# Kernel tuning notes

Hardware: AMD Instinct MI355X
Metric: run time of the kernel (lower is better)

The kernel has to match this reference:

```python
import jax, jax.numpy as jnp
import numpy as np
import math

D_MODEL = 512
N_HEADS = 8
D_K = D_MODEL // N_HEADS
B, S = 2, 4096
LN_EPS = 1e-5


def _xavier(key, fan_in, fan_out):
    limit = math.sqrt(6.0 / (fan_in + fan_out))
    return jax.random.uniform(key, (fan_in, fan_out), jnp.float32, -limit, limit)


def setup_inputs() -> dict:
    key = jax.random.key(0)
    ks = jax.random.split(key, 12)
    x = jax.random.normal(ks[0], (B, S, D_MODEL), jnp.float32)
    consciousness_state = jax.random.normal(ks[1], (B, D_MODEL), jnp.float32)
    # weights stored as [in, out] (equivalent to torch Linear weight.T)
    w_q = _xavier(ks[2], D_MODEL, D_MODEL)
    w_k = _xavier(ks[3], D_MODEL, D_MODEL)
    w_v = _xavier(ks[4], D_MODEL, D_MODEL)
    w_o = _xavier(ks[5], D_MODEL, D_MODEL)
    b_o = jnp.zeros((D_MODEL,), jnp.float32)
    w_gate = _xavier(ks[6], D_MODEL, N_HEADS)
    b_gate = jnp.zeros((N_HEADS,), jnp.float32)
    w_int = _xavier(ks[7], D_MODEL, D_MODEL)
    b_int = jnp.zeros((D_MODEL,), jnp.float32)
    ln_gamma = jnp.ones((D_MODEL,), jnp.float32)
    ln_beta = jnp.zeros((D_MODEL,), jnp.float32)
    return {"x": x, "consciousness_state": consciousness_state,
            "w_q": w_q, "w_k": w_k, "w_v": w_v, "w_o": w_o, "b_o": b_o,
            "w_gate": w_gate, "b_gate": b_gate, "w_int": w_int, "b_int": b_int,
            "ln_gamma": ln_gamma, "ln_beta": ln_beta}


def reference(x, consciousness_state, w_q, w_k, w_v, w_o, b_o,
              w_gate, b_gate, w_int, b_int, ln_gamma, ln_beta):
    b, s, d = x.shape
    # project and split heads: [B, H, S, d_k]
    def heads(w):
        return (x @ w).reshape(b, s, N_HEADS, D_K).transpose(0, 2, 1, 3)
    Q, K, V = heads(w_q), heads(w_k), heads(w_v)
    scores = jnp.einsum('bhsd,bhtd->bhst', Q, K) / math.sqrt(D_K)  # [B,H,S,S]
    # per-head consciousness gate BEFORE softmax
    cw = jax.nn.sigmoid(consciousness_state @ w_gate + b_gate)  # [B,H]
    scores = scores * cw[:, :, None, None]
    attn = jax.nn.softmax(scores, axis=-1)
    # dropout is identity in eval mode
    context = jnp.einsum('bhst,bhtd->bhsd', attn, V)
    context = context.transpose(0, 2, 1, 3).reshape(b, s, d)
    out = context @ w_o + b_o
    iw = jax.nn.sigmoid(consciousness_state @ w_int + b_int)  # [B,D]
    out = out * iw[:, None, :]
    # residual + LayerNorm
    h = out + x
    mu = jnp.mean(h, axis=-1, keepdims=True)
    var = jnp.var(h, axis=-1, keepdims=True)
    out = (h - mu) * jax.lax.rsqrt(var + LN_EPS) * ln_gamma + ln_beta
    return out, attn.mean(axis=1)
```

## Files before the change

### kernel.cpp

```cpp
#include <hip/hip_runtime.h>
#include <hip/hip_bf16.h>

using short8 = __attribute__((ext_vector_type(8))) short;
using f32x4  = __attribute__((ext_vector_type(4))) float;

#define S_LEN 4096
#define DM 512

__device__ __forceinline__ unsigned short f2b(float f) {
    unsigned int u = __float_as_uint(f);
    u += 0x7fffu + ((u >> 16) & 1u);
    return (unsigned short)(u >> 16);
}

__device__ __forceinline__ short8 pack8(float4 a, float4 b) {
    short8 r;
    r[0] = (short)f2b(a.x); r[1] = (short)f2b(a.y); r[2] = (short)f2b(a.z); r[3] = (short)f2b(a.w);
    r[4] = (short)f2b(b.x); r[5] = (short)f2b(b.y); r[6] = (short)f2b(b.z); r[7] = (short)f2b(b.w);
    return r;
}

__global__ __launch_bounds__(256) void convert_w(
    const float* __restrict__ w0, const float* __restrict__ w1,
    const float* __restrict__ w2, const float* __restrict__ w3,
    unsigned short* __restrict__ t0, unsigned short* __restrict__ t1,
    unsigned short* __restrict__ t2, unsigned short* __restrict__ t3)
{
    __shared__ float sh[64][65];
    const float* src; unsigned short* dst;
    switch (blockIdx.z) {
        case 0: src = w0; dst = t0; break;
        case 1: src = w1; dst = t1; break;
        case 2: src = w2; dst = t2; break;
        default: src = w3; dst = t3; break;
    }
    int k0 = blockIdx.x * 64, n0 = blockIdx.y * 64;
    int tid = threadIdx.x;
    for (int i = tid; i < 4096; i += 256) {
        int k = i >> 6, n = i & 63;
        sh[k][n] = src[(size_t)(k0 + k) * DM + n0 + n];
    }
    __syncthreads();
    for (int i = tid; i < 4096; i += 256) {
        int n = i >> 6, k = i & 63;
        dst[(size_t)(n0 + n) * DM + k0 + k] = f2b(sh[k][n]);
    }
}

__global__ __launch_bounds__(256) void convert_x(
    const float* __restrict__ x, unsigned short* __restrict__ xb)
{
    size_t i = ((size_t)blockIdx.x * 256 + threadIdx.x) * 8;
    float4 a = *reinterpret_cast<const float4*>(x + i);
    float4 b = *reinterpret_cast<const float4*>(x + i + 4);
    *reinterpret_cast<short8*>(xb + i) = pack8(a, b);
}

__global__ __launch_bounds__(64) void gates_kernel(
    const float* __restrict__ cs, const float* __restrict__ wg, const float* __restrict__ bg,
    const float* __restrict__ wi, const float* __restrict__ bi,
    float* __restrict__ cwout, float* __restrict__ iwout)
{
    int o = blockIdx.x, b = blockIdx.y, lane = threadIdx.x;
    const float* c = cs + (size_t)b * DM;
    float acc = 0.f;
    if (o < 8) {
        #pragma unroll
        for (int j = 0; j < 8; ++j) { int k = j * 64 + lane; acc += c[k] * wg[(size_t)k * 8 + o]; }
    } else {
        int n = o - 8;
        #pragma unroll
        for (int j = 0; j < 8; ++j) { int k = j * 64 + lane; acc += c[k] * wi[(size_t)k * DM + n]; }
    }
    #pragma unroll
    for (int d = 32; d; d >>= 1) acc += __shfl_xor(acc, d);
    if (lane == 0) {
        if (o < 8) cwout[b * 8 + o] = 1.f / (1.f + __expf(-(acc + bg[o])));
        else       iwout[b * DM + (o - 8)] = 1.f / (1.f + __expf(-(acc + bi[o - 8])));
    }
}

__global__ __launch_bounds__(256) void gemm_qkv(
    const unsigned short* __restrict__ A, const unsigned short* __restrict__ WT,
    const float* __restrict__ cw,
    unsigned short* __restrict__ Qb, unsigned short* __restrict__ Kb,
    unsigned short* __restrict__ Vt)
{
    __shared__ unsigned short a_sh[64][72];
    __shared__ unsigned short b_sh[64][72];
    const int m0 = blockIdx.x * 64;
    const int n0g = blockIdx.y * 64;
    const int which = blockIdx.y >> 3;
    const int tid = threadIdx.x;
    const int wave = tid >> 6, lane = tid & 63;
    const int g = lane >> 4, lr = lane & 15;
    const int srow = tid >> 3, skc = (tid & 7) * 8;

    float sq = 1.f;
    if (which == 0) {
        int b = blockIdx.x >> 6;
        int h = blockIdx.y & 7;
        sq = cw[b * 8 + h] * 0.125f * 1.44269504f;
    }

    f32x4 acc[4];
    #pragma unroll
    for (int i = 0; i < 4; ++i) acc[i] = (f32x4){0.f, 0.f, 0.f, 0.f};

    short8 ar[2], br[2];
    #pragma unroll
    for (int cc = 0; cc < 2; ++cc) {
        int row = srow + cc * 32;
        ar[cc] = *reinterpret_cast<const short8*>(A  + (size_t)(m0  + row) * DM + skc);
        br[cc] = *reinterpret_cast<const short8*>(WT + (size_t)(n0g + row) * DM + skc);
    }

    for (int k0 = 0; k0 < 512; k0 += 64) {
        #pragma unroll
        for (int cc = 0; cc < 2; ++cc) {
            int row = srow + cc * 32;
            *reinterpret_cast<short8*>(&a_sh[row][skc]) = ar[cc];
            *reinterpret_cast<short8*>(&b_sh[row][skc]) = br[cc];
        }
        __syncthreads();
        if (k0 + 64 < 512) {
            #pragma unroll
            for (int cc = 0; cc < 2; ++cc) {
                int row = srow + cc * 32;
                ar[cc] = *reinterpret_cast<const short8*>(A  + (size_t)(m0  + row) * DM + k0 + 64 + skc);
                br[cc] = *reinterpret_cast<const short8*>(WT + (size_t)(n0g + row) * DM + k0 + 64 + skc);
            }
        }
        __builtin_amdgcn_s_setprio(1);
        #pragma unroll
        for (int ks = 0; ks < 2; ++ks) {
            short8 af = *reinterpret_cast<const short8*>(&a_sh[wave * 16 + lr][ks * 32 + g * 8]);
            #pragma unroll
            for (int nf = 0; nf < 4; ++nf) {
                short8 bf = *reinterpret_cast<const short8*>(&b_sh[nf * 16 + lr][ks * 32 + g * 8]);
                acc[nf] = __builtin_amdgcn_mfma_f32_16x16x32_bf16(af, bf, acc[nf], 0, 0, 0);
            }
        }
        __builtin_amdgcn_s_setprio(0);
        __syncthreads();
    }

    #pragma unroll
    for (int nf = 0; nf < 4; ++nf) {
        #pragma unroll
        for (int r = 0; r < 4; ++r) {
            int m = m0 + wave * 16 + g * 4 + r;
            int nl = (blockIdx.y & 7) * 64 + nf * 16 + lr;
            unsigned short v = f2b(acc[nf][r] * sq);
            if (which == 0) {
                Qb[(size_t)m * DM + nl] = v;
            } else if (which == 1) {
                Kb[(size_t)m * DM + nl] = v;
            } else {
                int b = m >> 12, s = m & 4095;
                int h = nl >> 6, d = nl & 63;
                Vt[((size_t)(b * 8 + h) * 64 + d) * S_LEN + s] = v;
            }
        }
    }
}

__global__ __launch_bounds__(256) void gemm_proj(
    const unsigned short* __restrict__ A, const unsigned short* __restrict__ WT,
    float* __restrict__ outf, const float* __restrict__ bias,
    const float* __restrict__ iw, const float* __restrict__ xres)
{
    __shared__ unsigned short a_sh[64][72];
    __shared__ unsigned short b_sh[64][72];
    const int m0 = blockIdx.x * 64;
    const int n0 = blockIdx.y * 64;
    const int tid = threadIdx.x;
    const int wave = tid >> 6, lane = tid & 63;
    const int g = lane >> 4, lr = lane & 15;
    const int srow = tid >> 3, skc = (tid & 7) * 8;

    f32x4 acc[4];
    #pragma unroll
    for (int i = 0; i < 4; ++i) acc[i] = (f32x4){0.f, 0.f, 0.f, 0.f};

    short8 ar[2], br[2];
    #pragma unroll
    for (int cc = 0; cc < 2; ++cc) {
        int row = srow + cc * 32;
        ar[cc] = *reinterpret_cast<const short8*>(A  + (size_t)(m0 + row) * DM + skc);
        br[cc] = *reinterpret_cast<const short8*>(WT + (size_t)(n0 + row) * DM + skc);
    }

    for (int k0 = 0; k0 < 512; k0 += 64) {
        #pragma unroll
        for (int cc = 0; cc < 2; ++cc) {
            int row = srow + cc * 32;
            *reinterpret_cast<short8*>(&a_sh[row][skc]) = ar[cc];
            *reinterpret_cast<short8*>(&b_sh[row][skc]) = br[cc];
        }
        __syncthreads();
        if (k0 + 64 < 512) {
            #pragma unroll
            for (int cc = 0; cc < 2; ++cc) {
                int row = srow + cc * 32;
                ar[cc] = *reinterpret_cast<const short8*>(A  + (size_t)(m0 + row) * DM + k0 + 64 + skc);
                br[cc] = *reinterpret_cast<const short8*>(WT + (size_t)(n0 + row) * DM + k0 + 64 + skc);
            }
        }
        __builtin_amdgcn_s_setprio(1);
        #pragma unroll
        for (int ks = 0; ks < 2; ++ks) {
            short8 af = *reinterpret_cast<const short8*>(&a_sh[wave * 16 + lr][ks * 32 + g * 8]);
            #pragma unroll
            for (int nf = 0; nf < 4; ++nf) {
                short8 bf = *reinterpret_cast<const short8*>(&b_sh[nf * 16 + lr][ks * 32 + g * 8]);
                acc[nf] = __builtin_amdgcn_mfma_f32_16x16x32_bf16(af, bf, acc[nf], 0, 0, 0);
            }
        }
        __builtin_amdgcn_s_setprio(0);
        __syncthreads();
    }

    #pragma unroll
    for (int nf = 0; nf < 4; ++nf) {
        #pragma unroll
        for (int r = 0; r < 4; ++r) {
            int m = m0 + wave * 16 + g * 4 + r;
            int n = n0 + nf * 16 + lr;
            int b = m >> 12;
            float v = (acc[nf][r] + bias[n]) * iw[b * DM + n] + xres[(size_t)m * DM + n];
            outf[(size_t)m * DM + n] = v;
        }
    }
}

__global__ __launch_bounds__(256) void attn_ctx(
    const unsigned short* __restrict__ Qb, const unsigned short* __restrict__ Kb,
    const unsigned short* __restrict__ Vt,
    float* __restrict__ lbuf, unsigned short* __restrict__ ctx)
{
    __shared__ unsigned short k_sh[64][72];
    __shared__ unsigned short v_sh[64][72];
    __shared__ unsigned short p_sh[4][16][72];
    const int wg = blockIdx.x;
    const int logical = (wg & 7) * 128 + (wg >> 3);
    const int q0 = (logical & 63) * 64;
    const int bh = logical >> 6;
    const int b = bh >> 3, h = bh & 7;
    const int tid = threadIdx.x, wave = tid >> 6, lane = tid & 63;
    const int g = lane >> 4, lr = lane & 15;
    const int srow = tid >> 3, skc = (tid & 7) * 8;

    short8 qf[2];
    {
        const unsigned short* qp = Qb + (size_t)(b * S_LEN + q0 + wave * 16 + lr) * DM + h * 64;
        qf[0] = *reinterpret_cast<const short8*>(qp + g * 8);
        qf[1] = *reinterpret_cast<const short8*>(qp + 32 + g * 8);
    }
    short8 onesb;
    #pragma unroll
    for (int i = 0; i < 8; ++i) onesb[i] = (short)0x3F80;

    f32x4 lsum = (f32x4){0.f, 0.f, 0.f, 0.f};
    f32x4 cacc[4];
    #pragma unroll
    for (int i = 0; i < 4; ++i) cacc[i] = (f32x4){0.f, 0.f, 0.f, 0.f};

    const unsigned short* Kbase = Kb + (size_t)(b * S_LEN) * DM + h * 64;
    const unsigned short* Vbase = Vt + ((size_t)bh * 64) * S_LEN;

    short8 kr[2], vr[2];
    #pragma unroll
    for (int cc = 0; cc < 2; ++cc) {
        int row = srow + cc * 32;
        kr[cc] = *reinterpret_cast<const short8*>(Kbase + (size_t)row * DM + skc);
        vr[cc] = *reinterpret_cast<const short8*>(Vbase + (size_t)row * S_LEN + skc);
    }

    for (int kv0 = 0; kv0 < S_LEN; kv0 += 64) {
        #pragma unroll
        for (int cc = 0; cc < 2; ++cc) {
            int row = srow + cc * 32;
            *reinterpret_cast<short8*>(&k_sh[row][skc]) = kr[cc];
            *reinterpret_cast<short8*>(&v_sh[row][skc]) = vr[cc];
        }
        __syncthreads();
        f32x4 st[4];
        #pragma unroll
        for (int f = 0; f < 4; ++f) st[f] = (f32x4){0.f, 0.f, 0.f, 0.f};
        __builtin_amdgcn_s_setprio(1);
        #pragma unroll
        for (int ks = 0; ks < 2; ++ks) {
            #pragma unroll
            for (int f = 0; f < 4; ++f) {
                short8 kf = *reinterpret_cast<const short8*>(&k_sh[f * 16 + lr][ks * 32 + g * 8]);
                st[f] = __builtin_amdgcn_mfma_f32_16x16x32_bf16(kf, qf[ks], st[f], 0, 0, 0);
            }
        }
        __builtin_amdgcn_s_setprio(0);
        if (kv0 + 64 < S_LEN) {
            #pragma unroll
            for (int cc = 0; cc < 2; ++cc) {
                int row = srow + cc * 32;
                kr[cc] = *reinterpret_cast<const short8*>(Kbase + (size_t)(kv0 + 64 + row) * DM + skc);
                vr[cc] = *reinterpret_cast<const short8*>(Vbase + (size_t)row * S_LEN + kv0 + 64 + skc);
            }
        }
        #pragma unroll
        for (int f = 0; f < 4; ++f) {
            float p0 = __builtin_amdgcn_exp2f(st[f][0]);
            float p1 = __builtin_amdgcn_exp2f(st[f][1]);
            float p2 = __builtin_amdgcn_exp2f(st[f][2]);
            float p3 = __builtin_amdgcn_exp2f(st[f][3]);
            unsigned u0, u1;
            asm("v_cvt_pk_bf16_f32 %0, %1, %2" : "=v"(u0) : "v"(p0), "v"(p1));
            asm("v_cvt_pk_bf16_f32 %0, %1, %2" : "=v"(u1) : "v"(p2), "v"(p3));
            uint2 pv; pv.x = u0; pv.y = u1;
            *reinterpret_cast<uint2*>(&p_sh[wave][lr][f * 16 + g * 4]) = pv;
        }
        __builtin_amdgcn_s_setprio(1);
        #pragma unroll
        for (int ks = 0; ks < 2; ++ks) {
            short8 pf = *reinterpret_cast<const short8*>(&p_sh[wave][lr][ks * 32 + g * 8]);
            lsum = __builtin_amdgcn_mfma_f32_16x16x32_bf16(pf, onesb, lsum, 0, 0, 0);
            #pragma unroll
            for (int df = 0; df < 4; ++df) {
                short8 vf = *reinterpret_cast<const short8*>(&v_sh[df * 16 + lr][ks * 32 + g * 8]);
                cacc[df] = __builtin_amdgcn_mfma_f32_16x16x32_bf16(pf, vf, cacc[df], 0, 0, 0);
            }
        }
        __builtin_amdgcn_s_setprio(0);
        __syncthreads();
    }
    float rl[4];
    #pragma unroll
    for (int r = 0; r < 4; ++r) rl[r] = 1.f / lsum[r];
    if (lr == 0) {
        #pragma unroll
        for (int r = 0; r < 4; ++r)
            lbuf[bh * S_LEN + q0 + wave * 16 + g * 4 + r] = lsum[r];
    }
    #pragma unroll
    for (int df = 0; df < 4; ++df) {
        #pragma unroll
        for (int r = 0; r < 4; ++r) {
            int q = q0 + wave * 16 + g * 4 + r;
            ctx[(size_t)(b * S_LEN + q) * DM + h * 64 + df * 16 + lr] = f2b(cacc[df][r] * rl[r]);
        }
    }
}

__global__ __launch_bounds__(256) void attn_mean(
    const unsigned short* __restrict__ Qb, const unsigned short* __restrict__ Kb,
    const float* __restrict__ lbuf, float* __restrict__ outmean)
{
    __shared__ unsigned short k_sh[32][520];
    const int wg = blockIdx.x;
    const int logical = (wg & 7) * 128 + (wg >> 3);
    const int q0 = (logical & 63) * 64;
    const int kcb = logical >> 6;
    const int kc0 = (kcb & 7) * 512;
    const int b = kcb >> 3;
    const int tid = threadIdx.x, wave = tid >> 6, lane = tid & 63;
    const int g = lane >> 4, lr = lane & 15;
    const int srow = tid >> 6, scol = (tid & 63) * 8;

    float la2[8][4];
    #pragma unroll
    for (int h = 0; h < 8; ++h) {
        #pragma unroll
        for (int r = 0; r < 4; ++r) {
            int idx = (b * 8 + h) * S_LEN + q0 + wave * 16 + g * 4 + r;
            la2[h][r] = -log2f(lbuf[idx]) - 3.0f;
        }
    }
    const unsigned short* qbase = Qb + (size_t)(b * S_LEN + q0 + wave * 16 + lr) * DM;
    const unsigned short* Kbase = Kb + (size_t)(b * S_LEN) * DM;

    short8 stg[8];
    #pragma unroll
    for (int i = 0; i < 8; ++i) {
        int row = srow + i * 4;
        stg[i] = *reinterpret_cast<const short8*>(Kbase + (size_t)(kc0 + row) * DM + scol);
    }

    for (int t = 0; t < 16; ++t) {
        int kv0 = kc0 + t * 32;
        #pragma unroll
        for (int i = 0; i < 8; ++i) {
            int row = srow + i * 4;
            *reinterpret_cast<short8*>(&k_sh[row][scol]) = stg[i];
        }
        __syncthreads();
        if (t + 1 < 16) {
            #pragma unroll
            for (int i = 0; i < 8; ++i) {
                int row = srow + i * 4;
                stg[i] = *reinterpret_cast<const short8*>(Kbase + (size_t)(kv0 + 32 + row) * DM + scol);
            }
        }
        float macc[2][4];
        #pragma unroll
        for (int f = 0; f < 2; ++f)
            #pragma unroll
            for (int r = 0; r < 4; ++r) macc[f][r] = 0.f;
        #pragma unroll
        for (int h = 0; h < 8; ++h) {
            const unsigned short* qp = qbase + h * 64;
            short8 qf0 = *reinterpret_cast<const short8*>(qp + g * 8);
            short8 qf1 = *reinterpret_cast<const short8*>(qp + 32 + g * 8);
            f32x4 s[2];
            s[0] = (f32x4){0.f, 0.f, 0.f, 0.f};
            s[1] = (f32x4){0.f, 0.f, 0.f, 0.f};
            __builtin_amdgcn_s_setprio(1);
            #pragma unroll
            for (int f = 0; f < 2; ++f) {
                short8 kf0 = *reinterpret_cast<const short8*>(&k_sh[f * 16 + lr][h * 64 + g * 8]);
                s[f] = __builtin_amdgcn_mfma_f32_16x16x32_bf16(qf0, kf0, s[f], 0, 0, 0);
                short8 kf1 = *reinterpret_cast<const short8*>(&k_sh[f * 16 + lr][h * 64 + 32 + g * 8]);
                s[f] = __builtin_amdgcn_mfma_f32_16x16x32_bf16(qf1, kf1, s[f], 0, 0, 0);
            }
            __builtin_amdgcn_s_setprio(0);
            #pragma unroll
            for (int f = 0; f < 2; ++f)
                #pragma unroll
                for (int r = 0; r < 4; ++r)
                    macc[f][r] += __builtin_amdgcn_exp2f(s[f][r] + la2[h][r]);
        }
        #pragma unroll
        for (int f = 0; f < 2; ++f) {
            #pragma unroll
            for (int r = 0; r < 4; ++r) {
                int q = q0 + wave * 16 + g * 4 + r;
                outmean[(size_t)(b * S_LEN + q) * S_LEN + kv0 + f * 16 + lr] = macc[f][r];
            }
        }
        __syncthreads();
    }
}

__global__ __launch_bounds__(64) void ln_kernel(
    const float* __restrict__ hbuf, const float* __restrict__ gamma,
    const float* __restrict__ beta, float* __restrict__ dout)
{
    int row = blockIdx.x, lane = threadIdx.x;
    const float* hp = hbuf + (size_t)row * DM + lane * 8;
    float4 v0 = *reinterpret_cast<const float4*>(hp);
    float4 v1 = *reinterpret_cast<const float4*>(hp + 4);
    float s = v0.x + v0.y + v0.z + v0.w + v1.x + v1.y + v1.z + v1.w;
    float ss = v0.x * v0.x + v0.y * v0.y + v0.z * v0.z + v0.w * v0.w
             + v1.x * v1.x + v1.y * v1.y + v1.z * v1.z + v1.w * v1.w;
    #pragma unroll
    for (int d = 32; d; d >>= 1) { s += __shfl_xor(s, d); ss += __shfl_xor(ss, d); }
    float mu = s * (1.f / 512.f);
    float var = ss * (1.f / 512.f) - mu * mu;
    float rstd = rsqrtf(var + 1e-5f);
    float4 g0 = *reinterpret_cast<const float4*>(gamma + lane * 8);
    float4 g1 = *reinterpret_cast<const float4*>(gamma + lane * 8 + 4);
    float4 b0 = *reinterpret_cast<const float4*>(beta + lane * 8);
    float4 b1 = *reinterpret_cast<const float4*>(beta + lane * 8 + 4);
    float4 o0, o1;
    o0.x = (v0.x - mu) * rstd * g0.x + b0.x;
    o0.y = (v0.y - mu) * rstd * g0.y + b0.y;
    o0.z = (v0.z - mu) * rstd * g0.z + b0.z;
    o0.w = (v0.w - mu) * rstd * g0.w + b0.w;
    o1.x = (v1.x - mu) * rstd * g1.x + b1.x;
    o1.y = (v1.y - mu) * rstd * g1.y + b1.y;
    o1.z = (v1.z - mu) * rstd * g1.z + b1.z;
    o1.w = (v1.w - mu) * rstd * g1.w + b1.w;
    float* op = dout + (size_t)row * DM + lane * 8;
    *reinterpret_cast<float4*>(op) = o0;
    *reinterpret_cast<float4*>(op + 4) = o1;
}

extern "C" void kernel_launch(void* const* d_in, const int* in_sizes, int n_in,
                              void* d_out, int out_size, void* d_ws, size_t ws_size,
                              hipStream_t stream)
{
    const float* x   = (const float*)d_in[0];
    const float* cs  = (const float*)d_in[1];
    const float* wq  = (const float*)d_in[2];
    const float* wk  = (const float*)d_in[3];
    const float* wv  = (const float*)d_in[4];
    const float* wo  = (const float*)d_in[5];
    const float* bo  = (const float*)d_in[6];
    const float* wg  = (const float*)d_in[7];
    const float* bg  = (const float*)d_in[8];
    const float* wi  = (const float*)d_in[9];
    const float* bi  = (const float*)d_in[10];
    const float* gam = (const float*)d_in[11];
    const float* bet = (const float*)d_in[12];

    float* out = (float*)d_out;
    float* outmean = out + (size_t)2 * S_LEN * DM;

    char* ws = (char*)d_ws;
    size_t off = 0;
    auto alloc = [&](size_t bytes) { void* p = ws + off; off += (bytes + 255) & ~(size_t)255; return p; };

    unsigned short* wtq = (unsigned short*)alloc((size_t)DM * DM * 2);
    unsigned short* wtk = (unsigned short*)alloc((size_t)DM * DM * 2);
    unsigned short* wtv = (unsigned short*)alloc((size_t)DM * DM * 2);
    unsigned short* wto = (unsigned short*)alloc((size_t)DM * DM * 2);
    unsigned short* xb  = (unsigned short*)alloc((size_t)2 * S_LEN * DM * 2);
    unsigned short* Qb  = (unsigned short*)alloc((size_t)2 * S_LEN * DM * 2);
    unsigned short* Kb  = (unsigned short*)alloc((size_t)2 * S_LEN * DM * 2);
    unsigned short* Vt  = (unsigned short*)alloc((size_t)2 * S_LEN * DM * 2);
    unsigned short* ctx = (unsigned short*)alloc((size_t)2 * S_LEN * DM * 2);
    float* lbuf = (float*)alloc((size_t)16 * S_LEN * 4);
    float* cwb  = (float*)alloc(64);
    float* iwb  = (float*)alloc((size_t)2 * DM * 4);
    float* hbuf = (float*)Qb;

    convert_w<<<dim3(8, 8, 4), 256, 0, stream>>>(wq, wk, wv, wo, wtq, wtk, wtv, wto);
    convert_x<<<dim3(2048), 256, 0, stream>>>(x, xb);
    gates_kernel<<<dim3(520, 2), 64, 0, stream>>>(cs, wg, bg, wi, bi, cwb, iwb);

    gemm_qkv<<<dim3(128, 24), 256, 0, stream>>>(xb, wtq, cwb, Qb, Kb, Vt);

    attn_ctx<<<dim3(1024), 256, 0, stream>>>(Qb, Kb, Vt, lbuf, ctx);
    attn_mean<<<dim3(1024), 256, 0, stream>>>(Qb, Kb, lbuf, outmean);

    gemm_proj<<<dim3(128, 8), 256, 0, stream>>>(ctx, wto, hbuf, bo, iwb, x);
    ln_kernel<<<dim3(2 * S_LEN), 64, 0, stream>>>(hbuf, gam, bet, out);
}
```

Baseline: 271.8 us.

## Split attention KV range in two and combine partials in a new kernel

The attention-context kernel now splits each query tile's KV sequence into two halves, launching twice as many workgroups. Each half writes unnormalized fp32 partial context and row sums to a scratch buffer. A new combine kernel adds the two halves, normalizes, writes the row sums and bf16 context. The aim is better occupancy across CUs (1024 blocks may not fill 256 CUs evenly). The cost is an extra launch and roughly 34MB of fp32 scratch traffic. No max subtraction is needed because scores are pre-scaled without a running max.

Result: slower. 281.6 us (+3.6%).

```diff
diff --git a/kernel.cpp b/kernel.cpp
--- a/kernel.cpp
+++ b/kernel.cpp
@@ -236,17 +236,19 @@
 
 __global__ __launch_bounds__(256) void attn_ctx(
     const unsigned short* __restrict__ Qb, const unsigned short* __restrict__ Kb,
-    const unsigned short* __restrict__ Vt,
-    float* __restrict__ lbuf, unsigned short* __restrict__ ctx)
+    const unsigned short* __restrict__ Vt, float* __restrict__ pacc)
 {
     __shared__ unsigned short k_sh[64][72];
     __shared__ unsigned short v_sh[64][72];
     __shared__ unsigned short p_sh[4][16][72];
     const int wg = blockIdx.x;
-    const int logical = (wg & 7) * 128 + (wg >> 3);
-    const int q0 = (logical & 63) * 64;
-    const int bh = logical >> 6;
+    const int logical = (wg & 7) * 256 + (wg >> 3);
+    const int qt = logical & 63;
+    const int s = (logical >> 6) & 1;
+    const int bh = logical >> 7;
+    const int q0 = qt * 64;
     const int b = bh >> 3, h = bh & 7;
+    const int kvbeg = s * 2048, kvend = kvbeg + 2048;
     const int tid = threadIdx.x, wave = tid >> 6, lane = tid & 63;
     const int g = lane >> 4, lr = lane & 15;
     const int srow = tid >> 3, skc = (tid & 7) * 8;
@@ -273,11 +275,11 @@
     #pragma unroll
     for (int cc = 0; cc < 2; ++cc) {
         int row = srow + cc * 32;
-        kr[cc] = *reinterpret_cast<const short8*>(Kbase + (size_t)row * DM + skc);
-        vr[cc] = *reinterpret_cast<const short8*>(Vbase + (size_t)row * S_LEN + skc);
-    }
-
-    for (int kv0 = 0; kv0 < S_LEN; kv0 += 64) {
+        kr[cc] = *reinterpret_cast<const short8*>(Kbase + (size_t)(kvbeg + row) * DM + skc);
+        vr[cc] = *reinterpret_cast<const short8*>(Vbase + (size_t)row * S_LEN + kvbeg + skc);
+    }
+
+    for (int kv0 = kvbeg; kv0 < kvend; kv0 += 64) {
         #pragma unroll
         for (int cc = 0; cc < 2; ++cc) {
             int row = srow + cc * 32;
@@ -298,7 +300,7 @@
             }
         }
         __builtin_amdgcn_s_setprio(0);
-        if (kv0 + 64 < S_LEN) {
+        if (kv0 + 64 < kvend) {
             #pragma unroll
             for (int cc = 0; cc < 2; ++cc) {
                 int row = srow + cc * 32;
@@ -332,22 +334,47 @@
         __builtin_amdgcn_s_setprio(0);
         __syncthreads();
     }
-    float rl[4];
-    #pragma unroll
-    for (int r = 0; r < 4; ++r) rl[r] = 1.f / lsum[r];
+    float* pb = pacc + (size_t)logical * 4160;
+    #pragma unroll
+    for (int df = 0; df < 4; ++df) {
+        #pragma unroll
+        for (int r = 0; r < 4; ++r)
+            pb[(wave * 16 + g * 4 + r) * 64 + df * 16 + lr] = cacc[df][r];
+    }
     if (lr == 0) {
         #pragma unroll
         for (int r = 0; r < 4; ++r)
-            lbuf[bh * S_LEN + q0 + wave * 16 + g * 4 + r] = lsum[r];
-    }
-    #pragma unroll
-    for (int df = 0; df < 4; ++df) {
-        #pragma unroll
-        for (int r = 0; r < 4; ++r) {
-            int q = q0 + wave * 16 + g * 4 + r;
-            ctx[(size_t)(b * S_LEN + q) * DM + h * 64 + df * 16 + lr] = f2b(cacc[df][r] * rl[r]);
-        }
-    }
+            pb[4096 + wave * 16 + g * 4 + r] = lsum[r];
+    }
+}
+
+__global__ __launch_bounds__(256) void attn_combine(
+    const float* __restrict__ pacc, float* __restrict__ lbuf,
+    unsigned short* __restrict__ ctx)
+{
+    const int L = blockIdx.x;
+    const int bh = L >> 6, qt = L & 63;
+    const int b = bh >> 3, h = bh & 7;
+    const float* P0 = pacc + (size_t)(bh * 128 + qt) * 4160;
+    const float* P1 = pacc + (size_t)(bh * 128 + 64 + qt) * 4160;
+    const int tid = threadIdx.x;
+    const int q = tid >> 2, d0 = (tid & 3) * 16;
+    float l = P0[4096 + q] + P1[4096 + q];
+    if ((tid & 3) == 0) lbuf[bh * S_LEN + qt * 64 + q] = l;
+    float rl = 1.f / l;
+    unsigned short tmp[16];
+    #pragma unroll
+    for (int i = 0; i < 16; i += 4) {
+        float4 a = *reinterpret_cast<const float4*>(P0 + q * 64 + d0 + i);
+        float4 c = *reinterpret_cast<const float4*>(P1 + q * 64 + d0 + i);
+        tmp[i]     = f2b((a.x + c.x) * rl);
+        tmp[i + 1] = f2b((a.y + c.y) * rl);
+        tmp[i + 2] = f2b((a.z + c.z) * rl);
+        tmp[i + 3] = f2b((a.w + c.w) * rl);
+    }
+    unsigned short* cp = ctx + (size_t)(b * S_LEN + qt * 64 + q) * DM + h * 64 + d0;
+    *reinterpret_cast<short8*>(cp)     = *reinterpret_cast<short8*>(tmp);
+    *reinterpret_cast<short8*>(cp + 8) = *reinterpret_cast<short8*>(tmp + 8);
 }
 
 __global__ __launch_bounds__(256) void attn_mean(
@@ -510,6 +537,7 @@
     float* lbuf = (float*)alloc((size_t)16 * S_LEN * 4);
     float* cwb  = (float*)alloc(64);
     float* iwb  = (float*)alloc((size_t)2 * DM * 4);
+    float* pacc = (float*)alloc((size_t)2048 * 4160 * 4);
     float* hbuf = (float*)Qb;
 
     convert_w<<<dim3(8, 8, 4), 256, 0, stream>>>(wq, wk, wv, wo, wtq, wtk, wtv, wto);
@@ -518,7 +546,8 @@
 
     gemm_qkv<<<dim3(128, 24), 256, 0, stream>>>(xb, wtq, cwb, Qb, Kb, Vt);
 
-    attn_ctx<<<dim3(1024), 256, 0, stream>>>(Qb, Kb, Vt, lbuf, ctx);
+    attn_ctx<<<dim3(2048), 256, 0, stream>>>(Qb, Kb, Vt, pacc);
+    attn_combine<<<dim3(1024), 256, 0, stream>>>(pacc, lbuf, ctx);
     attn_mean<<<dim3(1024), 256, 0, stream>>>(Qb, Kb, lbuf, outmean);
 
     gemm_proj<<<dim3(128, 8), 256, 0, stream>>>(ctx, wto, hbuf, bo, iwb, x);
```
